# Kernel tuning notes

Measured on AMD Instinct MI355X. Metric: run time of the kernel, lower is better.

## Reference

```python
import jax, jax.numpy as jnp
import numpy as np
import math

B, N, H, C = 1, 2048, 8, 128
PQ, PV, R, CS, CZ = 8, 12, 2, 256, 128
CZ4 = CZ // 4
INF = 1e5
EPS = 1e-8
SOFTPLUS_INV_1 = 0.541324854612918


def _quat_to_rot(q):
    q = q / jnp.linalg.norm(q, axis=-1, keepdims=True)
    w, x, y, z = q[..., 0], q[..., 1], q[..., 2], q[..., 3]
    return jnp.stack([
        jnp.stack([1 - 2 * (y * y + z * z), 2 * (x * y - z * w), 2 * (x * z + y * w)], -1),
        jnp.stack([2 * (x * y + z * w), 1 - 2 * (x * x + z * z), 2 * (y * z - x * w)], -1),
        jnp.stack([2 * (x * z - y * w), 2 * (y * z + x * w), 1 - 2 * (x * x + y * y)], -1),
    ], -2)


def setup_inputs() -> dict:
    key = jax.random.key(0)
    ks = jax.random.split(key, 16)
    rn = lambda k, shape, s=1.0: jax.random.normal(k, shape, dtype=jnp.float32) * s
    hc = H * C
    return dict(
        s=rn(ks[0], (B, N, CS)),
        z_factor_1=rn(ks[1], (B, N, R, CZ)),
        z_factor_2=rn(ks[2], (B, N, R, CZ)),
        rot=_quat_to_rot(rn(ks[3], (B, N, 4))),
        trans=rn(ks[4], (B, N, 3)),
        mask=jnp.ones((B, N), dtype=bool),
        w_q=rn(ks[5], (hc, CS), 0.02), b_q=jnp.zeros((hc,), jnp.float32),
        w_kv=rn(ks[6], (2 * hc, CS), 0.02), b_kv=jnp.zeros((2 * hc,), jnp.float32),
        w_qp=rn(ks[7], (H * PQ * 3, CS), 0.02), b_qp=jnp.zeros((H * PQ * 3,), jnp.float32),
        w_kvp=rn(ks[8], (H * (PQ + PV) * 3, CS), 0.02), b_kvp=jnp.zeros((H * (PQ + PV) * 3,), jnp.float32),
        w_b=rn(ks[9], (H, CZ), 0.02), b_b=jnp.zeros((H,), jnp.float32),
        w_dz=rn(ks[10], (CZ4, CZ), 0.02), b_dz=jnp.zeros((CZ4,), jnp.float32),
        head_weights=jnp.full((H,), SOFTPLUS_INV_1, dtype=jnp.float32),
        w_out=rn(ks[11], (CS, H * (CZ4 + C + 4 * PV)), 0.02), b_out=jnp.zeros((CS,), jnp.float32),
    )


def _lin(x, w, b):
    return x @ w.T + b


def _ipa(s, z1, z2, rot, trans, mask, w_q, b_q, w_kv, b_kv, w_qp, b_qp,
         w_kvp, b_kvp, w_b, b_b, w_dz, b_dz, head_weights, w_out, b_out):
    q = _lin(s, w_q, b_q).reshape(B, N, H, C)
    kv = _lin(s, w_kv, b_kv).reshape(B, N, H, 2 * C)
    k, v = kv[..., :C], kv[..., C:]
    # local points -> global frame: x_glob = R x_loc + t
    qp = _lin(s, w_qp, b_qp).reshape(B, N, H * PQ, 3)
    qp = (jnp.einsum('bnij,bnpj->bnpi', rot, qp) + trans[:, :, None, :]).reshape(B, N, H, PQ, 3)
    kvp = _lin(s, w_kvp, b_kvp).reshape(B, N, H * (PQ + PV), 3)
    kvp = (jnp.einsum('bnij,bnpj->bnpi', rot, kvp) + trans[:, :, None, :]).reshape(B, N, H, PQ + PV, 3)
    kp, vp = kvp[..., :PQ, :], kvp[..., PQ:, :]
    # head weights: softplus init to 1, AF2 scaling sqrt(1/(3*(PQ*9/2)))
    hw = jax.nn.softplus(head_weights) * math.sqrt(1.0 / (3 * (PQ * 9.0 / 2)))
    # low-rank pair bias factors
    b1 = _lin(z1, w_b, b_b)   # [B,N,R,H]
    b2 = _lin(z2, w_b, b_b)
    z1d = _lin(z1, w_dz, b_dz)  # [B,N,R,CZ4]
    z2d = _lin(z2, w_dz, b_dz)
    # logits: scalar QK + point-distance + low-rank pair bias
    scalar = jnp.einsum('bihc,bjhc->bhij', q, k) * math.sqrt(1.0 / (3 * C))
    ptdot = jnp.einsum('bihpx,bjhpx->bhij', qp, kp)
    qn = jnp.sum(qp * qp, axis=(-1, -2))  # [B,N,H]
    kn = jnp.sum(kp * kp, axis=(-1, -2))
    pt_term = hw[None, :, None, None] * (
        ptdot - 0.5 * qn.transpose(0, 2, 1)[:, :, :, None] - 0.5 * kn.transpose(0, 2, 1)[:, :, None, :])
    pair = jnp.einsum('birh,bjrh->bhij', b1, b2)
    mask_bias = jnp.where(mask, 0.0, -INF)[:, None, None, :]
    a = jax.nn.softmax(scalar + pt_term + pair + mask_bias, axis=-1)  # [B,H,N,N]
    # outputs
    o = jnp.einsum('bhij,bjhc->bihc', a, v).reshape(B, N, H * C)
    opt = jnp.einsum('bhij,bjhpx->bihpx', a, vp)  # global-frame points
    opt_loc = jnp.einsum('bnji,bnhpj->bnhpi', rot, opt - trans[:, :, None, None, :])  # R^T (x - t)
    opt_norm = jnp.sqrt(jnp.sum(opt_loc * opt_loc, axis=-1) + EPS)  # [B,N,H,PV]
    oz = jnp.einsum('bhij,bjrc->bihrc', a, z2d)
    opair = jnp.sum(oz * z1d[:, :, None, :, :], axis=3)  # [B,N,H,CZ4]
    feats = jnp.concatenate([
        o,
        opt_loc[..., 0].reshape(B, N, H * PV),
        opt_loc[..., 1].reshape(B, N, H * PV),
        opt_loc[..., 2].reshape(B, N, H * PV),
        opt_norm.reshape(B, N, H * PV),
        opair.reshape(B, N, H * CZ4),
    ], axis=-1)
    return _lin(feats, w_out, b_out)  # [B,N,CS]


def reference(s, z_factor_1, z_factor_2, rot, trans, mask, w_q, b_q, w_kv, b_kv,
              w_qp, b_qp, w_kvp, b_kvp, w_b, b_b, w_dz, b_dz, head_weights,
              w_out, b_out):
    return _ipa(s, z_factor_1, z_factor_2, rot, trans, mask, w_q, b_q, w_kv, b_kv,
                w_qp, b_qp, w_kvp, b_kvp, w_b, b_b, w_dz, b_dz, head_weights,
                w_out, b_out)
```

## Files before the change

### kernel.cpp

```cpp
#include <hip/hip_runtime.h>
#include <math.h>

#define NN   2048
#define HH   8
#define CC   128
#define PQn  8
#define PVn  12
#define RRn  2
#define CSn  256
#define CZn  128
#define CZ4n 32
#define HC   (HH*CC)
#define FEAT (HC + 4*HH*PVn + HH*CZ4n)
#define DA   160
#define DVP  256
#define DVU  240
#define QKV  3840
#define LOG2E 1.4426950408889634f

typedef unsigned short ushort_t;
#define AS1 __attribute__((address_space(1)))
#define AS3 __attribute__((address_space(3)))

using bfrag = __attribute__((ext_vector_type(8))) short;
using ffrag = __attribute__((ext_vector_type(4))) float;

__device__ inline ushort_t f2bf(float x) {
    union { float f; unsigned int u; } v; v.f = x;
    unsigned int r = v.u + 0x7fffu + ((v.u >> 16) & 1u);
    return (ushort_t)(r >> 16);
}
__device__ inline float bf2f(ushort_t x) {
    union { unsigned int u; float f; } v; v.u = ((unsigned int)x) << 16; return v.f;
}

struct CvtArgs {
    const float4* src[12];
    ushort4* dst[12];
    int n4[12];
};
__global__ __launch_bounds__(256) void cvtn_kernel(CvtArgs a,
    float4* __restrict__ outp, const float4* __restrict__ bias4)
{
    int i = blockIdx.x * 256 + threadIdx.x;
    if (i < NN * CSn / 4) {
        outp[i] = bias4[i & 63];
        return;
    }
    i -= NN * CSn / 4;
#pragma unroll
    for (int k = 0; k < 12; ++k) {
        if (i < a.n4[k]) {
            ushort4 o;
            if (a.src[k]) {
                float4 v = a.src[k][i];
                o = make_ushort4(f2bf(v.x), f2bf(v.y), f2bf(v.z), f2bf(v.w));
            } else {
                o = make_ushort4(0, 0, 0, 0);
            }
            a.dst[k][i] = o;
            return;
        }
        i -= a.n4[k];
    }
}

__global__ __launch_bounds__(256) void bgemm_kernel(
    const ushort_t* __restrict__ A, size_t sA,
    const ushort_t* __restrict__ B, size_t sB,
    void* __restrict__ Cv, size_t sC,
    const float* __restrict__ bias, size_t sBias,
    int ldk, int kOff, int kOffPerZ, int kLen, int ldc, int obf, int atomicOut)
{
    const int z = blockIdx.z;
    A += (size_t)z * sA;
    B += (size_t)z * sB;
    const float* bp = bias ? (bias + (size_t)z * sBias) : nullptr;
    const int k0beg = kOff + z * kOffPerZ;
    const int r0 = blockIdx.y * 128;
    const int c0 = blockIdx.x * 128;
    __shared__ __align__(16) ushort_t lA[128 * 32];
    __shared__ __align__(16) ushort_t lB[128 * 32];
    const int tid = threadIdx.x;
    const int w = tid >> 6, lane = tid & 63;
    const int wm = (w >> 1) * 64, wn = (w & 1) * 64;
    const int lrA = lane >> 2;
    const int lcA = (lane & 3) * 8;
    ffrag acc[4][4] = {};

    for (int k0 = k0beg; k0 < k0beg + kLen; k0 += 32) {
#pragma unroll
        for (int t = 0; t < 2; ++t) {
            int instr = w * 2 + t;
            int r = instr * 16 + lrA;
            const ushort_t* ga = A + (size_t)(r0 + r) * ldk + k0 + lcA;
            const ushort_t* gb = B + (size_t)(c0 + r) * ldk + k0 + lcA;
            __builtin_amdgcn_global_load_lds((const AS1 void*)ga,
                (AS3 void*)((AS3 ushort_t*)&lA[instr * 512 + lane * 8]), 16, 0, 0);
            __builtin_amdgcn_global_load_lds((const AS1 void*)gb,
                (AS3 void*)((AS3 ushort_t*)&lB[instr * 512 + lane * 8]), 16, 0, 0);
        }
        __syncthreads();
        bfrag af[4], bf[4];
#pragma unroll
        for (int mi = 0; mi < 4; ++mi)
            af[mi] = *(const bfrag*)&lA[(wm + mi * 16 + (lane & 15)) * 32 + (lane >> 4) * 8];
#pragma unroll
        for (int ni = 0; ni < 4; ++ni)
            bf[ni] = *(const bfrag*)&lB[(wn + ni * 16 + (lane & 15)) * 32 + (lane >> 4) * 8];
#pragma unroll
        for (int mi = 0; mi < 4; ++mi)
#pragma unroll
            for (int ni = 0; ni < 4; ++ni)
                acc[mi][ni] = __builtin_amdgcn_mfma_f32_16x16x32_bf16(af[mi], bf[ni], acc[mi][ni], 0, 0, 0);
        __syncthreads();
    }
#pragma unroll
    for (int mi = 0; mi < 4; ++mi) {
#pragma unroll
        for (int ni = 0; ni < 4; ++ni) {
            int col = c0 + wn + ni * 16 + (lane & 15);
            float bv = bp ? bp[col] : 0.f;
#pragma unroll
            for (int rr = 0; rr < 4; ++rr) {
                int row = r0 + wm + mi * 16 + (lane >> 4) * 4 + rr;
                float val = acc[mi][ni][rr] + bv;
                if (atomicOut)
                    unsafeAtomicAdd(&((float*)Cv)[(size_t)z * sC + (size_t)row * ldc + col], val);
                else if (obf)
                    ((ushort_t*)Cv)[(size_t)z * sC + (size_t)row * ldc + col] = f2bf(val);
                else
                    ((float*)Cv)[(size_t)z * sC + (size_t)row * ldc + col] = val;
            }
        }
    }
}

__global__ __launch_bounds__(256) void mgemm_kernel(
    const ushort_t* __restrict__ A0, const ushort_t* __restrict__ B0,
    ushort_t* __restrict__ C0,
    const ushort_t* __restrict__ A1, const ushort_t* __restrict__ B1,
    ushort_t* __restrict__ C1)
{
    const int bx = blockIdx.x;
    const ushort_t *A, *B;
    ushort_t* C;
    int ldk, kLen, ldc, r0, c0;
    if (bx < 480) {
        A = A0; B = B0; C = C0;
        ldk = CSn; kLen = CSn; ldc = QKV;
        r0 = (bx / 30) * 128;
        c0 = (bx % 30) * 128;
    } else {
        int i = bx - 480;
        A = A1; B = B1; C = C1;
        ldk = CZn; kLen = CZn; ldc = 128;
        r0 = i * 128;
        c0 = 0;
    }
    __shared__ __align__(16) ushort_t lA[128 * 32];
    __shared__ __align__(16) ushort_t lB[128 * 32];
    const int tid = threadIdx.x;
    const int w = tid >> 6, lane = tid & 63;
    const int wm = (w >> 1) * 64, wn = (w & 1) * 64;
    const int lrA = lane >> 2;
    const int lcA = (lane & 3) * 8;
    ffrag acc[4][4] = {};

    for (int k0 = 0; k0 < kLen; k0 += 32) {
#pragma unroll
        for (int t = 0; t < 2; ++t) {
            int instr = w * 2 + t;
            int r = instr * 16 + lrA;
            const ushort_t* ga = A + (size_t)(r0 + r) * ldk + k0 + lcA;
            const ushort_t* gb = B + (size_t)(c0 + r) * ldk + k0 + lcA;
            __builtin_amdgcn_global_load_lds((const AS1 void*)ga,
                (AS3 void*)((AS3 ushort_t*)&lA[instr * 512 + lane * 8]), 16, 0, 0);
            __builtin_amdgcn_global_load_lds((const AS1 void*)gb,
                (AS3 void*)((AS3 ushort_t*)&lB[instr * 512 + lane * 8]), 16, 0, 0);
        }
        __syncthreads();
        bfrag af[4], bf[4];
#pragma unroll
        for (int mi = 0; mi < 4; ++mi)
            af[mi] = *(const bfrag*)&lA[(wm + mi * 16 + (lane & 15)) * 32 + (lane >> 4) * 8];
#pragma unroll
        for (int ni = 0; ni < 4; ++ni)
            bf[ni] = *(const bfrag*)&lB[(wn + ni * 16 + (lane & 15)) * 32 + (lane >> 4) * 8];
#pragma unroll
        for (int mi = 0; mi < 4; ++mi)
#pragma unroll
            for (int ni = 0; ni < 4; ++ni)
                acc[mi][ni] = __builtin_amdgcn_mfma_f32_16x16x32_bf16(af[mi], bf[ni], acc[mi][ni], 0, 0, 0);
        __syncthreads();
    }
#pragma unroll
    for (int mi = 0; mi < 4; ++mi) {
#pragma unroll
        for (int ni = 0; ni < 4; ++ni) {
            int col = c0 + wn + ni * 16 + (lane & 15);
#pragma unroll
            for (int rr = 0; rr < 4; ++rr) {
                int row = r0 + wm + mi * 16 + (lane >> 4) * 4 + rr;
                C[(size_t)row * ldc + col] = f2bf(acc[mi][ni][rr]);
            }
        }
    }
}

__global__ __launch_bounds__(256) void prep_kernel(
    const ushort_t* __restrict__ qkv,
    const ushort_t* __restrict__ zproj,
    const float* __restrict__ b_q, const float* __restrict__ b_kv,
    const float* __restrict__ b_qp, const float* __restrict__ b_kvp,
    const float* __restrict__ b_b, const float* __restrict__ b_dz,
    const float* __restrict__ rot, const float* __restrict__ trans,
    const float* __restrict__ hwts,
    ushort_t* __restrict__ qaug, ushort_t* __restrict__ kaug,
    ushort_t* __restrict__ vaug)
{
    const int i = blockIdx.x;
    const int tid = threadIdx.x;
    __shared__ float R[9], t[3];
    __shared__ float qp_l[192], kp_l[192], vp_l[288];
    __shared__ float kn_s[8], hw_s[8];
    __shared__ __align__(16) ushort_t qa_s[8 * DA];
    __shared__ __align__(16) ushort_t ka_s[8 * DA];
    __shared__ __align__(16) ushort_t va_s[8 * DVP];
    if (tid < 9) R[tid] = rot[i*9 + tid];
    if (tid < 3) t[tid] = trans[i*3 + tid];
    if (tid < 8) {
        hw_s[tid] = log1pf(expf(hwts[tid])) * 0.09622504486493763f;
        kn_s[tid] = 0.f;
    }
    __syncthreads();
    if (tid < 64) {
        const ushort_t* v = qkv + (size_t)i*QKV + 3072 + tid*3;
        float vx = bf2f(v[0]) + b_qp[tid*3+0];
        float vy = bf2f(v[1]) + b_qp[tid*3+1];
        float vz = bf2f(v[2]) + b_qp[tid*3+2];
        float X = R[0]*vx + R[1]*vy + R[2]*vz + t[0];
        float Y = R[3]*vx + R[4]*vy + R[5]*vz + t[1];
        float Z = R[6]*vx + R[7]*vy + R[8]*vz + t[2];
        qp_l[tid*3+0] = X; qp_l[tid*3+1] = Y; qp_l[tid*3+2] = Z;
    } else if (tid < 224) {
        int p = tid - 64;
        int h = p / 20, pp = p % 20;
        const ushort_t* v = qkv + (size_t)i*QKV + 3264 + p*3;
        float vx = bf2f(v[0]) + b_kvp[p*3+0];
        float vy = bf2f(v[1]) + b_kvp[p*3+1];
        float vz = bf2f(v[2]) + b_kvp[p*3+2];
        float X = R[0]*vx + R[1]*vy + R[2]*vz + t[0];
        float Y = R[3]*vx + R[4]*vy + R[5]*vz + t[1];
        float Z = R[6]*vx + R[7]*vy + R[8]*vz + t[2];
        if (pp < 8) {
            int b = (h*8 + pp) * 3;
            kp_l[b+0] = X; kp_l[b+1] = Y; kp_l[b+2] = Z;
            atomicAdd(&kn_s[h], X*X + Y*Y + Z*Z);
        } else {
            int b = (h*12 + pp - 8) * 3;
            vp_l[b+0] = X; vp_l[b+1] = Y; vp_l[b+2] = Z;
        }
    }
    __syncthreads();

    const float QS = 0.05103103630798288f * LOG2E;
    for (int idx = tid; idx < 8 * DA; idx += 256) {
        int h = idx / DA, d = idx - h * DA;
        float qv, kv2;
        if (d < 128) {
            qv  = QS * (bf2f(qkv[(size_t)i*QKV + h*128 + d]) + b_q[h*128 + d]);
            kv2 = bf2f(qkv[(size_t)i*QKV + 1024 + h*256 + d]) + b_kv[h*256 + d];
        } else if (d < 152) {
            qv  = hw_s[h] * LOG2E * qp_l[h*24 + d - 128];
            kv2 = kp_l[h*24 + d - 128];
        } else if (d < 154) {
            int r = d - 152;
            qv  = LOG2E * (bf2f(zproj[(size_t)(i*2 + r)*128 + h]) + b_b[h]);
            kv2 = bf2f(zproj[(size_t)(4096 + i*2 + r)*128 + h]) + b_b[h];
        } else if (d == 154) {
            qv  = LOG2E;
            kv2 = -0.5f * hw_s[h] * kn_s[h];
        } else { qv = 0.f; kv2 = 0.f; }
        qa_s[idx] = f2bf(qv);
        ka_s[idx] = f2bf(kv2);
    }
    for (int idx = tid; idx < 8 * DVP; idx += 256) {
        int h = idx >> 8, d = idx & 255;
        float v;
        if (d < 128)       v = bf2f(qkv[(size_t)i*QKV + 1024 + h*256 + 128 + d]) + b_kv[h*256 + 128 + d];
        else if (d < 164)  v = vp_l[h*36 + d - 128];
        else if (d < 196)  v = bf2f(zproj[(size_t)(4096 + i*2 + 0)*128 + 8 + d - 164]) + b_dz[d - 164];
        else if (d < 228)  v = bf2f(zproj[(size_t)(4096 + i*2 + 1)*128 + 8 + d - 196]) + b_dz[d - 196];
        else if (d == 239) v = 1.0f;
        else               v = 0.f;
        va_s[idx] = f2bf(v);
    }
    __syncthreads();

    for (int idx = tid; idx < 576; idx += 256) {
        if (idx < 160) {
            int h = idx / 20, dg = (idx - h*20) * 8;
            *(bfrag*)(qaug + ((size_t)h*NN + i) * DA + dg) = *(const bfrag*)&qa_s[h*DA + dg];
        } else if (idx < 320) {
            int r = idx - 160;
            int h = r / 20, dg = (r - h*20) * 8;
            *(bfrag*)(kaug + ((size_t)h*NN + i) * DA + dg) = *(const bfrag*)&ka_s[h*DA + dg];
        } else {
            int r = idx - 320;
            int h = r >> 5, dg = (r & 31) * 8;
            *(bfrag*)(vaug + ((size_t)h*NN + i) * DVP + dg) = *(const bfrag*)&va_s[h*DVP + dg];
        }
    }
}

__global__ __launch_bounds__(256) void transpose_kernel(
    const ushort_t* __restrict__ in, ushort_t* __restrict__ out)
{
    const int z = blockIdx.z;
    in  += (size_t)z * NN * DVP;
    out += (size_t)z * NN * DVP;
    const int i0 = blockIdx.x * 64;
    const int d0 = blockIdx.y * 64;
    __shared__ __align__(8) ushort_t tb[64][72];
    const int tid = threadIdx.x;
#pragma unroll
    for (int p = 0; p < 4; ++p) {
        int idx = p * 256 + tid;
        int r = idx >> 4, sg = idx & 15;
        ushort4 v = *(const ushort4*)(in + (size_t)(i0 + r) * DVP + d0 + sg * 4);
        *(ushort4*)&tb[r][sg * 4] = v;
    }
    __syncthreads();
#pragma unroll
    for (int p = 0; p < 4; ++p) {
        int idx = p * 256 + tid;
        int d = idx >> 4, ig = idx & 15;
        ushort4 v = make_ushort4(tb[ig*4+0][d], tb[ig*4+1][d],
                                 tb[ig*4+2][d], tb[ig*4+3][d]);
        *(ushort4*)(out + (size_t)(d0 + d) * NN + i0 + ig * 4) = v;
    }
}

__global__ __launch_bounds__(1024, 4) void flash_kernel(
    const ushort_t* __restrict__ qaug,
    const ushort_t* __restrict__ kaug,
    const ushort_t* __restrict__ vaugT,
    ushort_t* __restrict__ Opart,
    float* __restrict__ Mpart,
    float* __restrict__ Lpart)
{
    const int bid = blockIdx.x;
    const int G = bid & 15;
    const int m = bid >> 4;
    const int h = G >> 1;
    const int g = G & 1;
    const int i0 = m * 128;

    __shared__ __align__(16) ushort_t Kt[2][64 * 168];
    __shared__ __align__(16) ushort_t Vt[2][DVU * 72];
    __shared__ __align__(16) ushort_t Pl[2][128 * 72];

    const int tid = threadIdx.x;
    const int w = tid >> 6, lane = tid & 63;
    const int quad = lane >> 4, lc = lane & 15;
    const int rq = w >> 1, jq = w & 1;
    const int rh = w >> 2, dh = (w >> 1) & 1, jc = w & 1;

    const ushort_t* qh = qaug + (size_t)h * NN * DA;
    const ushort_t* kh = kaug + (size_t)h * NN * DA;
    const ushort_t* vh = vaugT + (size_t)h * DVP * NN;

    const int j0g = g * 1024;
    const int iK0 = tid, iK1 = 1024 + tid;
    const int rK0 = iK0 / 21, oK0 = iK0 - rK0 * 21;
    const int rK1 = iK1 / 21, oK1 = iK1 - rK1 * 21;
    const bool vK1 = (tid < 320);
    const ushort_t* kS0 = kh + (size_t)(j0g + rK0) * DA + (oK0 < 20 ? oK0 * 8 : 0);
    const ushort_t* kS1 = kh + (size_t)(j0g + rK1) * DA + (oK1 < 20 ? oK1 * 8 : 0);
    const int iV0 = tid, iV1 = 1024 + tid, iV2 = 2048 + tid;
    const int rV0 = iV0 / 9, oV0 = iV0 - rV0 * 9;
    const int rV1 = iV1 / 9, oV1 = iV1 - rV1 * 9;
    const int rV2 = iV2 / 9, oV2 = iV2 - rV2 * 9;
    const bool vV2 = (tid < 112);
    const ushort_t* vS0 = vh + (size_t)rV0 * NN + j0g + (oV0 < 8 ? oV0 * 8 : 0);
    const ushort_t* vS1 = vh + (size_t)rV1 * NN + j0g + (oV1 < 8 ? oV1 * 8 : 0);
    const ushort_t* vS2 = vh + (size_t)(vV2 ? rV2 : 0) * NN + j0g + (oV2 < 8 ? oV2 * 8 : 0);

    auto stageK = [&](ushort_t* dst) {
        __builtin_amdgcn_global_load_lds((const AS1 void*)kS0,
            (AS3 void*)((AS3 ushort_t*)&dst[iK0 * 8]), 16, 0, 0);
        if (vK1)
            __builtin_amdgcn_global_load_lds((const AS1 void*)kS1,
                (AS3 void*)((AS3 ushort_t*)&dst[iK1 * 8]), 16, 0, 0);
        kS0 += 64 * DA; kS1 += 64 * DA;
    };
    auto stageV = [&](ushort_t* dst) {
        __builtin_amdgcn_global_load_lds((const AS1 void*)vS0,
            (AS3 void*)((AS3 ushort_t*)&dst[iV0 * 8]), 16, 0, 0);
        __builtin_amdgcn_global_load_lds((const AS1 void*)vS1,
            (AS3 void*)((AS3 ushort_t*)&dst[iV1 * 8]), 16, 0, 0);
        if (vV2)
            __builtin_amdgcn_global_load_lds((const AS1 void*)vS2,
                (AS3 void*)((AS3 ushort_t*)&dst[iV2 * 8]), 16, 0, 0);
        vS0 += 64; vS1 += 64; vS2 += 64;
    };

    bfrag qf[5];
#pragma unroll
    for (int ks = 0; ks < 5; ++ks)
        qf[ks] = *(const bfrag*)(qh + (size_t)(i0 + rq * 16 + lc) * DA + ks * 32 + quad * 8);

    ffrag acc[2][8];
#pragma unroll
    for (int mi = 0; mi < 2; ++mi)
#pragma unroll
        for (int t = 0; t < 8; ++t)
            acc[mi][t] = (ffrag){0.f, 0.f, 0.f, 0.f};

    stageK(Kt[0]);
    stageV(Vt[0]);
    __syncthreads();

    for (int it = 0; it < 16; ++it) {
        const int cur = it & 1;

        if (it < 15) stageK(Kt[cur ^ 1]);

        ffrag sf[2];
        sf[0] = (ffrag){0.f, 0.f, 0.f, 0.f};
        sf[1] = (ffrag){0.f, 0.f, 0.f, 0.f};
        const ushort_t* ktb = &Kt[cur][(jq * 32 + lc) * 168 + quad * 8];
        __builtin_amdgcn_s_setprio(1);
#pragma unroll
        for (int ks = 0; ks < 5; ++ks) {
            bfrag kf0 = *(const bfrag*)(ktb + ks * 32);
            bfrag kf1 = *(const bfrag*)(ktb + 16 * 168 + ks * 32);
            sf[0] = __builtin_amdgcn_mfma_f32_16x16x32_bf16(qf[ks], kf0, sf[0], 0, 0, 0);
            sf[1] = __builtin_amdgcn_mfma_f32_16x16x32_bf16(qf[ks], kf1, sf[1], 0, 0, 0);
        }

        if (it > 0) {
            const ushort_t* Plp = Pl[cur ^ 1];
            bfrag pf0 = *(const bfrag*)&Plp[(rh * 32 + lc) * 72 + jc * 32 + quad * 8];
            bfrag pf1 = *(const bfrag*)&Plp[(rh * 32 + 16 + lc) * 72 + jc * 32 + quad * 8];
            const ushort_t* vtb = &Vt[cur ^ 1][(dh * 128 + lc) * 72 + jc * 32 + quad * 8];
#pragma unroll
            for (int t = 0; t < 8; ++t) {
                if (dh && t == 7) continue;
                bfrag vf = *(const bfrag*)(vtb + t * 16 * 72);
                acc[0][t] = __builtin_amdgcn_mfma_f32_16x16x32_bf16(pf0, vf, acc[0][t], 0, 0, 0);
                acc[1][t] = __builtin_amdgcn_mfma_f32_16x16x32_bf16(pf1, vf, acc[1][t], 0, 0, 0);
            }
        }
        __builtin_amdgcn_s_setprio(0);

        {
            ushort_t* Plc = Pl[cur];
#pragma unroll
            for (int jt = 0; jt < 2; ++jt)
#pragma unroll
                for (int rr = 0; rr < 4; ++rr)
                    Plc[(rq * 16 + quad * 4 + rr) * 72 + jq * 32 + jt * 16 + lc] =
                        f2bf(exp2f(sf[jt][rr]));
        }

        __syncthreads();

        if (it < 15) stageV(Vt[cur ^ 1]);
    }

    {
        const ushort_t* Plp = Pl[1];
        bfrag pf0 = *(const bfrag*)&Plp[(rh * 32 + lc) * 72 + jc * 32 + quad * 8];
        bfrag pf1 = *(const bfrag*)&Plp[(rh * 32 + 16 + lc) * 72 + jc * 32 + quad * 8];
        const ushort_t* vtb = &Vt[1][(dh * 128 + lc) * 72 + jc * 32 + quad * 8];
#pragma unroll
        for (int t = 0; t < 8; ++t) {
            if (dh && t == 7) continue;
            bfrag vf = *(const bfrag*)(vtb + t * 16 * 72);
            acc[0][t] = __builtin_amdgcn_mfma_f32_16x16x32_bf16(pf0, vf, acc[0][t], 0, 0, 0);
            acc[1][t] = __builtin_amdgcn_mfma_f32_16x16x32_bf16(pf1, vf, acc[1][t], 0, 0, 0);
        }
    }

    const int part = g * 2 + jc;
    ushort_t* Ob = Opart + ((size_t)part * HH + h) * NN * DVU;
#pragma unroll
    for (int mi = 0; mi < 2; ++mi)
#pragma unroll
        for (int t = 0; t < 8; ++t) {
            if (dh && t == 7) continue;
            int dt = dh * 8 + t;
#pragma unroll
            for (int rr = 0; rr < 4; ++rr) {
                int row = i0 + rh * 32 + mi * 16 + quad * 4 + rr;
                Ob[(size_t)row * DVU + dt * 16 + lc] = f2bf(acc[mi][t][rr]);
            }
        }
    size_t sb = ((size_t)part * HH + h) * NN;
    if (dh == 0 && lane < 32)
        Mpart[sb + i0 + rh * 32 + lane] = 0.f;
    if (dh == 1 && lc == 15) {
#pragma unroll
        for (int mi = 0; mi < 2; ++mi)
#pragma unroll
            for (int rr = 0; rr < 4; ++rr)
                Lpart[sb + i0 + rh * 32 + mi * 16 + quad * 4 + rr] = acc[mi][6][rr];
    }
}

__global__ __launch_bounds__(256) void combine_kernel(
    const ushort_t* __restrict__ Opart, const float* __restrict__ Mpart,
    const float* __restrict__ Lpart, const ushort_t* __restrict__ zproj,
    const float* __restrict__ b_dz,
    const float* __restrict__ rot, const float* __restrict__ trans,
    ushort_t* __restrict__ feats)
{
    const int i = blockIdx.x;
    const int tid = threadIdx.x;
    __shared__ float wgt[4][8];
    __shared__ float Ol[8][DVU];
    if (tid < 8) {
        int h = tid;
        float mm[4], ll[4];
#pragma unroll
        for (int p = 0; p < 4; ++p) {
            mm[p] = Mpart[((size_t)p * HH + h) * NN + i];
            ll[p] = Lpart[((size_t)p * HH + h) * NN + i];
        }
        float M = fmaxf(fmaxf(mm[0], mm[1]), fmaxf(mm[2], mm[3]));
        float Z = 0.f, e[4];
#pragma unroll
        for (int p = 0; p < 4; ++p) { e[p] = exp2f(mm[p] - M); Z += ll[p] * e[p]; }
        float zi = 1.f / Z;
#pragma unroll
        for (int p = 0; p < 4; ++p) wgt[p][h] = e[p] * zi;
    }
    __syncthreads();
    {
        int h = tid >> 5;
        int dg0 = tid & 31;
        for (int dg = dg0; dg < 60; dg += 32) {
            int d = dg * 4;
            float vx = 0.f, vy = 0.f, vz = 0.f, vw = 0.f;
#pragma unroll
            for (int p = 0; p < 4; ++p) {
                ushort4 u = *(const ushort4*)&Opart[(((size_t)p * HH + h) * NN + i) * DVU + d];
                float wv = wgt[p][h];
                vx += bf2f(u.x) * wv; vy += bf2f(u.y) * wv;
                vz += bf2f(u.z) * wv; vw += bf2f(u.w) * wv;
            }
            Ol[h][d] = vx; Ol[h][d+1] = vy; Ol[h][d+2] = vz; Ol[h][d+3] = vw;
        }
    }
    __syncthreads();

    ushort_t* f = feats + (size_t)i * FEAT;
    {
        int h = tid >> 5;
        int c = (tid * 4) & 127;
        ushort4 o4 = make_ushort4(f2bf(Ol[h][c]), f2bf(Ol[h][c+1]),
                                  f2bf(Ol[h][c+2]), f2bf(Ol[h][c+3]));
        *(ushort4*)(f + tid * 4) = o4;
    }
    if (tid < 96) {
        int h = tid / 12, p = tid % 12;
        const float* Rm = rot + i * 9;
        float ox = Ol[h][128 + p*3 + 0] - trans[i*3 + 0];
        float oy = Ol[h][128 + p*3 + 1] - trans[i*3 + 1];
        float oz = Ol[h][128 + p*3 + 2] - trans[i*3 + 2];
        float lx = Rm[0]*ox + Rm[3]*oy + Rm[6]*oz;
        float ly = Rm[1]*ox + Rm[4]*oy + Rm[7]*oz;
        float lz = Rm[2]*ox + Rm[5]*oy + Rm[8]*oz;
        float nrm = sqrtf(lx*lx + ly*ly + lz*lz + 1e-8f);
        f[1024 + 0*96 + tid] = f2bf(lx);
        f[1024 + 1*96 + tid] = f2bf(ly);
        f[1024 + 2*96 + tid] = f2bf(lz);
        f[1024 + 3*96 + tid] = f2bf(nrm);
    }
    {
        int h = tid >> 5, c = tid & 31;
        float z1d0 = bf2f(zproj[(size_t)(i*2 + 0)*128 + 8 + c]) + b_dz[c];
        float z1d1 = bf2f(zproj[(size_t)(i*2 + 1)*128 + 8 + c]) + b_dz[c];
        f[1408 + tid] = f2bf(Ol[h][164 + c] * z1d0 + Ol[h][196 + c] * z1d1);
    }
}

extern "C" void kernel_launch(void* const* d_in, const int* in_sizes, int n_in,
                              void* d_out, int out_size, void* d_ws, size_t ws_size,
                              hipStream_t stream) {
    const float* s     = (const float*)d_in[0];
    const float* z1    = (const float*)d_in[1];
    const float* z2    = (const float*)d_in[2];
    const float* rot   = (const float*)d_in[3];
    const float* trans = (const float*)d_in[4];
    const float* w_q   = (const float*)d_in[6];
    const float* b_q   = (const float*)d_in[7];
    const float* w_kv  = (const float*)d_in[8];
    const float* b_kv  = (const float*)d_in[9];
    const float* w_qp  = (const float*)d_in[10];
    const float* b_qp  = (const float*)d_in[11];
    const float* w_kvp = (const float*)d_in[12];
    const float* b_kvp = (const float*)d_in[13];
    const float* w_b   = (const float*)d_in[14];
    const float* b_b   = (const float*)d_in[15];
    const float* w_dz  = (const float*)d_in[16];
    const float* b_dz  = (const float*)d_in[17];
    const float* hwts  = (const float*)d_in[18];
    const float* w_out = (const float*)d_in[19];
    const float* b_out = (const float*)d_in[20];
    float* out = (float*)d_out;

    char* base = (char*)d_ws;
    const size_t OPART_BYTES = (size_t)4*HH*NN*DVU*2;
    char* S = base;
    ushort_t* s_bf  = (ushort_t*)(S);
    ushort_t* z_bf  = (ushort_t*)(S + 1048576);
    ushort_t* wall  = (ushort_t*)(S + 1048576 + 2097152);
    ushort_t* wz    = (ushort_t*)(S + 1048576 + 2097152 + 1966080);
    ushort_t* qkv   = (ushort_t*)(S + 1048576 + 2097152 + 1966080 + 32768);
    ushort_t* vaug  = (ushort_t*)(S + 1048576 + 2097152 + 1966080 + 32768 + 15728640);
    ushort_t* Opart = (ushort_t*)(S);
    char* P = base + OPART_BYTES;
    size_t off = 0;
    auto alloc = [&](size_t bytes) -> void* {
        void* p = P + off;
        off += (bytes + 255) & ~(size_t)255;
        return p;
    };
    ushort_t* wout_bf = (ushort_t*)alloc((size_t)CSn*FEAT*2);
    ushort_t* zproj   = (ushort_t*)alloc((size_t)8192*128*2);
    ushort_t* qaug    = (ushort_t*)alloc((size_t)HH*NN*DA*2);
    ushort_t* kaug    = (ushort_t*)alloc((size_t)HH*NN*DA*2);
    ushort_t* vaugT   = (ushort_t*)alloc((size_t)HH*NN*DVP*2);
    float*    Mpart   = (float*)alloc((size_t)4*HH*NN*4);
    float*    Lpart   = (float*)alloc((size_t)4*HH*NN*4);
    ushort_t* feats   = (ushort_t*)alloc((size_t)NN*FEAT*2);

    CvtArgs ca;
    int j = 0; int tot = 0;
    auto job = [&](const float* src, ushort_t* dst, int nElem) {
        ca.src[j] = (const float4*)src; ca.dst[j] = (ushort4*)dst; ca.n4[j] = nElem/4;
        tot += nElem/4; ++j;
    };
    job(s,     s_bf,              NN*CSn);
    job(z1,    z_bf,              4096*128);
    job(z2,    z_bf + 4096*128,   4096*128);
    job(w_q,   wall,              1024*256);
    job(w_kv,  wall + 1024*256,   2048*256);
    job(w_qp,  wall + 3072*256,   192*256);
    job(w_kvp, wall + 3264*256,   480*256);
    job(w_out, wout_bf,           CSn*FEAT);
    job(nullptr, wall + 3744*256, 96*256);
    job(w_b,   wz,                8*128);
    job(w_dz,  wz + 8*128,        32*128);
    job(nullptr, wz + 40*128,     88*128);
    tot += NN*CSn/4;
    cvtn_kernel<<<(tot + 255)/256, 256, 0, stream>>>(ca, (float4*)out, (const float4*)b_out);

    mgemm_kernel<<<544, 256, 0, stream>>>(s_bf, wall, qkv, z_bf, wz, zproj);

    prep_kernel<<<NN, 256, 0, stream>>>(qkv, zproj,
                                        b_q, b_kv, b_qp, b_kvp, b_b, b_dz,
                                        rot, trans, hwts, qaug, kaug, vaug);
    transpose_kernel<<<dim3(NN/64, DVP/64, HH), 256, 0, stream>>>(vaug, vaugT);

    flash_kernel<<<256, 1024, 0, stream>>>(
        qaug, kaug, vaugT, Opart, Mpart, Lpart);

    combine_kernel<<<NN, 256, 0, stream>>>(Opart, Mpart, Lpart, zproj, b_dz,
                                           rot, trans, feats);

    bgemm_kernel<<<dim3(CSn/128, NN/128, 4), 256, 0, stream>>>(
        feats, 0, wout_bf, 0, out, 0, nullptr, 0,
        FEAT, 0, FEAT/4, FEAT/4, CSn, 0, 1);
}
```

Baseline: 202.6 us.

## Reduce flash partials in-block via LDS and vectorize prep loads

Each flash block now sums the two column-split (jc) partial accumulators through shared memory before writing, so only two partials per head go to global memory instead of four. The unused Mpart max buffer is dropped, and the combine kernel now just sums two partials and divides by the summed L. The prep kernel also loads q/k/v channels as 8-wide bf16 vectors instead of scalar loads. The goal is less global write and read traffic for partials. The cost is extra LDS round-trips and barriers at the end of the flash kernel, plus a bf16 rounding of one partial before it is added.

```diff
diff --git a/kernel.cpp b/kernel.cpp
--- a/kernel.cpp
+++ b/kernel.cpp
@@ -265,13 +265,23 @@
     __syncthreads();
 
     const float QS = 0.05103103630798288f * LOG2E;
-    for (int idx = tid; idx < 8 * DA; idx += 256) {
-        int h = idx / DA, d = idx - h * DA;
+    if (tid < 128) {
+        int h = tid >> 4, d = (tid & 15) * 8;
+        bfrag q8 = *(const bfrag*)(qkv + (size_t)i*QKV + h*128 + d);
+        bfrag k8 = *(const bfrag*)(qkv + (size_t)i*QKV + 1024 + h*256 + d);
+        ushort_t qo[8], ko[8];
+#pragma unroll
+        for (int e = 0; e < 8; ++e) {
+            qo[e] = f2bf(QS * (bf2f((ushort_t)q8[e]) + b_q[h*128 + d + e]));
+            ko[e] = f2bf(bf2f((ushort_t)k8[e]) + b_kv[h*256 + d + e]);
+        }
+        *(bfrag*)&qa_s[h*DA + d] = *(bfrag*)qo;
+        *(bfrag*)&ka_s[h*DA + d] = *(bfrag*)ko;
+    }
+    {
+        int h = tid >> 5, d = 128 + (tid & 31);
         float qv, kv2;
-        if (d < 128) {
-            qv  = QS * (bf2f(qkv[(size_t)i*QKV + h*128 + d]) + b_q[h*128 + d]);
-            kv2 = bf2f(qkv[(size_t)i*QKV + 1024 + h*256 + d]) + b_kv[h*256 + d];
-        } else if (d < 152) {
+        if (d < 152) {
             qv  = hw_s[h] * LOG2E * qp_l[h*24 + d - 128];
             kv2 = kp_l[h*24 + d - 128];
         } else if (d < 154) {
@@ -282,19 +292,29 @@
             qv  = LOG2E;
             kv2 = -0.5f * hw_s[h] * kn_s[h];
         } else { qv = 0.f; kv2 = 0.f; }
-        qa_s[idx] = f2bf(qv);
-        ka_s[idx] = f2bf(kv2);
-    }
-    for (int idx = tid; idx < 8 * DVP; idx += 256) {
-        int h = idx >> 8, d = idx & 255;
+        qa_s[h*DA + d] = f2bf(qv);
+        ka_s[h*DA + d] = f2bf(kv2);
+    }
+    if (tid < 128) {
+        int h = tid >> 4, d = (tid & 15) * 8;
+        bfrag v8 = *(const bfrag*)(qkv + (size_t)i*QKV + 1024 + h*256 + 128 + d);
+        ushort_t vo[8];
+#pragma unroll
+        for (int e = 0; e < 8; ++e)
+            vo[e] = f2bf(bf2f((ushort_t)v8[e]) + b_kv[h*256 + 128 + d + e]);
+        *(bfrag*)&va_s[h*DVP + d] = *(bfrag*)vo;
+    }
+#pragma unroll
+    for (int k = 0; k < 4; ++k) {
+        int idx = k * 256 + tid;
+        int h = idx >> 7, d = 128 + (idx & 127);
         float v;
-        if (d < 128)       v = bf2f(qkv[(size_t)i*QKV + 1024 + h*256 + 128 + d]) + b_kv[h*256 + 128 + d];
-        else if (d < 164)  v = vp_l[h*36 + d - 128];
+        if (d < 164)       v = vp_l[h*36 + d - 128];
         else if (d < 196)  v = bf2f(zproj[(size_t)(4096 + i*2 + 0)*128 + 8 + d - 164]) + b_dz[d - 164];
         else if (d < 228)  v = bf2f(zproj[(size_t)(4096 + i*2 + 1)*128 + 8 + d - 196]) + b_dz[d - 196];
         else if (d == 239) v = 1.0f;
         else               v = 0.f;
-        va_s[idx] = f2bf(v);
+        va_s[h*DVP + d] = f2bf(v);
     }
     __syncthreads();
 
@@ -347,7 +367,6 @@
     const ushort_t* __restrict__ kaug,
     const ushort_t* __restrict__ vaugT,
     ushort_t* __restrict__ Opart,
-    float* __restrict__ Mpart,
     float* __restrict__ Lpart)
 {
     const int bid = blockIdx.x;
@@ -484,58 +503,71 @@
         }
     }
 
-    const int part = g * 2 + jc;
-    ushort_t* Ob = Opart + ((size_t)part * HH + h) * NN * DVU;
-#pragma unroll
-    for (int mi = 0; mi < 2; ++mi)
-#pragma unroll
-        for (int t = 0; t < 8; ++t) {
-            if (dh && t == 7) continue;
-            int dt = dh * 8 + t;
-#pragma unroll
-            for (int rr = 0; rr < 4; ++rr) {
-                int row = i0 + rh * 32 + mi * 16 + quad * 4 + rr;
-                Ob[(size_t)row * DVU + dt * 16 + lc] = f2bf(acc[mi][t][rr]);
+    ushort_t* scratch = (ushort_t*)Vt;
+    const int pw = w >> 1;
+    __syncthreads();
+    if (jc == 1) {
+        ushort_t tmp[64];
+#pragma unroll
+        for (int mi = 0; mi < 2; ++mi)
+#pragma unroll
+            for (int t = 0; t < 8; ++t)
+#pragma unroll
+                for (int rr = 0; rr < 4; ++rr)
+                    tmp[mi*32 + t*4 + rr] = f2bf(acc[mi][t][rr]);
+#pragma unroll
+        for (int j = 0; j < 8; ++j)
+            *(bfrag*)&scratch[pw * 4096 + j * 512 + lane * 8] = *(bfrag*)&tmp[j * 8];
+    }
+    __syncthreads();
+    if (jc == 0) {
+#pragma unroll
+        for (int j = 0; j < 8; ++j) {
+            bfrag v = *(const bfrag*)&scratch[pw * 4096 + j * 512 + lane * 8];
+#pragma unroll
+            for (int e = 0; e < 8; ++e) {
+                int idx = j * 8 + e;
+                acc[idx >> 5][(idx >> 2) & 7][idx & 3] += bf2f((ushort_t)v[e]);
             }
         }
-    size_t sb = ((size_t)part * HH + h) * NN;
-    if (dh == 0 && lane < 32)
-        Mpart[sb + i0 + rh * 32 + lane] = 0.f;
-    if (dh == 1 && lc == 15) {
+        ushort_t* Ob = Opart + ((size_t)g * HH + h) * NN * DVU;
 #pragma unroll
         for (int mi = 0; mi < 2; ++mi)
 #pragma unroll
-            for (int rr = 0; rr < 4; ++rr)
-                Lpart[sb + i0 + rh * 32 + mi * 16 + quad * 4 + rr] = acc[mi][6][rr];
+            for (int t = 0; t < 8; ++t) {
+                if (dh && t == 7) continue;
+                int dt = dh * 8 + t;
+#pragma unroll
+                for (int rr = 0; rr < 4; ++rr) {
+                    int row = i0 + rh * 32 + mi * 16 + quad * 4 + rr;
+                    Ob[(size_t)row * DVU + dt * 16 + lc] = f2bf(acc[mi][t][rr]);
+                }
+            }
+        size_t sb = ((size_t)g * HH + h) * NN;
+        if (dh == 1 && lc == 15) {
+#pragma unroll
+            for (int mi = 0; mi < 2; ++mi)
+#pragma unroll
+                for (int rr = 0; rr < 4; ++rr)
+                    Lpart[sb + i0 + rh * 32 + mi * 16 + quad * 4 + rr] = acc[mi][6][rr];
+        }
     }
 }
 
 __global__ __launch_bounds__(256) void combine_kernel(
-    const ushort_t* __restrict__ Opart, const float* __restrict__ Mpart,
-    const float* __restrict__ Lpart, const ushort_t* __restrict__ zproj,
-    const float* __restrict__ b_dz,
+    const ushort_t* __restrict__ Opart, const float* __restrict__ Lpart,
+    const ushort_t* __restrict__ zproj, const float* __restrict__ b_dz,
     const float* __restrict__ rot, const float* __restrict__ trans,
     ushort_t* __restrict__ feats)
 {
     const int i = blockIdx.x;
     const int tid = threadIdx.x;
-    __shared__ float wgt[4][8];
+    __shared__ float wgt8[8];
     __shared__ float Ol[8][DVU];
     if (tid < 8) {
-        int h = tid;
-        float mm[4], ll[4];
-#pragma unroll
-        for (int p = 0; p < 4; ++p) {
-            mm[p] = Mpart[((size_t)p * HH + h) * NN + i];
-            ll[p] = Lpart[((size_t)p * HH + h) * NN + i];
-        }
-        float M = fmaxf(fmaxf(mm[0], mm[1]), fmaxf(mm[2], mm[3]));
-        float Z = 0.f, e[4];
-#pragma unroll
-        for (int p = 0; p < 4; ++p) { e[p] = exp2f(mm[p] - M); Z += ll[p] * e[p]; }
-        float zi = 1.f / Z;
-#pragma unroll
-        for (int p = 0; p < 4; ++p) wgt[p][h] = e[p] * zi;
+        float l0 = Lpart[(size_t)(0 * HH + tid) * NN + i];
+        float l1 = Lpart[(size_t)(1 * HH + tid) * NN + i];
+        wgt8[tid] = 1.f / (l0 + l1);
     }
     __syncthreads();
     {
@@ -543,15 +575,13 @@
         int dg0 = tid & 31;
         for (int dg = dg0; dg < 60; dg += 32) {
             int d = dg * 4;
-            float vx = 0.f, vy = 0.f, vz = 0.f, vw = 0.f;
-#pragma unroll
-            for (int p = 0; p < 4; ++p) {
-                ushort4 u = *(const ushort4*)&Opart[(((size_t)p * HH + h) * NN + i) * DVU + d];
-                float wv = wgt[p][h];
-                vx += bf2f(u.x) * wv; vy += bf2f(u.y) * wv;
-                vz += bf2f(u.z) * wv; vw += bf2f(u.w) * wv;
-            }
-            Ol[h][d] = vx; Ol[h][d+1] = vy; Ol[h][d+2] = vz; Ol[h][d+3] = vw;
+            ushort4 u0 = *(const ushort4*)&Opart[(((size_t)0 * HH + h) * NN + i) * DVU + d];
+            ushort4 u1 = *(const ushort4*)&Opart[(((size_t)1 * HH + h) * NN + i) * DVU + d];
+            float wv = wgt8[h];
+            Ol[h][d+0] = (bf2f(u0.x) + bf2f(u1.x)) * wv;
+            Ol[h][d+1] = (bf2f(u0.y) + bf2f(u1.y)) * wv;
+            Ol[h][d+2] = (bf2f(u0.z) + bf2f(u1.z)) * wv;
+            Ol[h][d+3] = (bf2f(u0.w) + bf2f(u1.w)) * wv;
         }
     }
     __syncthreads();
@@ -637,6 +667,7 @@
     float*    Mpart   = (float*)alloc((size_t)4*HH*NN*4);
     float*    Lpart   = (float*)alloc((size_t)4*HH*NN*4);
     ushort_t* feats   = (ushort_t*)alloc((size_t)NN*FEAT*2);
+    (void)Mpart;
 
     CvtArgs ca;
     int j = 0; int tot = 0;
@@ -667,9 +698,9 @@
     transpose_kernel<<<dim3(NN/64, DVP/64, HH), 256, 0, stream>>>(vaug, vaugT);
 
     flash_kernel<<<256, 1024, 0, stream>>>(
-        qaug, kaug, vaugT, Opart, Mpart, Lpart);
-
-    combine_kernel<<<NN, 256, 0, stream>>>(Opart, Mpart, Lpart, zproj, b_dz,
+        qaug, kaug, vaugT, Opart, Lpart);
+
+    combine_kernel<<<NN, 256, 0, stream>>>(Opart, Lpart, zproj, b_dz,
                                            rot, trans, feats);
 
     bgemm_kernel<<<dim3(CSn/128, NN/128, 4), 256, 0, stream>>>(
```

After: 194.0 us. 1.04x faster.
